# Kernel optimization log

Hardware: AMD Instinct MI355X
Metric: run time of the kernel (lower is better)

The kernel has to match this reference:

```python
import jax, jax.numpy as jnp
import numpy as np

B, N = 8, 256
IN_F, OUT_F = 64, 64
IN_E, OUT_E = 32, 64  # out_edges must equal out_features (batched matmul constraint)


def setup_inputs() -> dict:
    key = jax.random.key(0)
    ks = jax.random.split(key, 9)
    s = 0.05
    return {
        "A": jax.random.uniform(ks[0], (B, N, N), dtype=jnp.float32),
        "emb_node": jax.random.normal(ks[1], (B, N, IN_F), dtype=jnp.float32),
        "emb_edge": jax.random.normal(ks[2], (B, N, N, IN_E), dtype=jnp.float32),
        "W_node": jax.random.normal(ks[3], (IN_F, OUT_F), dtype=jnp.float32) * s,
        "b_node": jnp.zeros((OUT_F,), dtype=jnp.float32),
        "W_nodes": jax.random.normal(ks[4], (IN_F, OUT_F), dtype=jnp.float32) * s,
        "b_nodes": jnp.zeros((OUT_F,), dtype=jnp.float32),
        "W_edge": jax.random.normal(ks[5], (IN_E, OUT_E), dtype=jnp.float32) * s,
        "b_edge": jnp.zeros((OUT_E,), dtype=jnp.float32),
    }


def reference(A, emb_node, emb_edge, W_node, b_node, W_nodes, b_nodes, W_edge, b_edge):
    # Dense projections (last-axis matmul, like keras Dense)
    node_x = emb_node @ W_node + b_node        # [B,N,F]
    node_sx = emb_node @ W_nodes + b_nodes     # [B,N,F]
    edge_x = emb_edge @ W_edge + b_edge        # [B,N,N,E] (E == F)
    # Fused edge-weighted aggregation: original materializes A[...,None]*edge_x
    # then does a per-channel batched matmul with node_x; same math as:
    #   node_out[b,n,f] = sum_m A[b,n,m] * edge_x[b,n,m,f] * node_x[b,m,f]
    agg = jnp.einsum('bnm,bnmf,bmf->bnf', A, edge_x, node_x)
    node_out = jax.nn.relu(agg) + jax.nn.relu(node_sx)
    edge_out = jax.nn.relu(edge_x)
    return node_out, edge_out
```

## Files before the change

### kernel.cpp

```cpp
#include <hip/hip_runtime.h>

#define BB    8
#define NN    256
#define OUTF  64
#define INE   32

using f4 = __attribute__((ext_vector_type(4))) float;

__device__ float g_node_x[BB * NN * OUTF];
__device__ float g_relu_sx[BB * NN * OUTF];

__global__ __launch_bounds__(256) void node_proj(
    const float* __restrict__ emb_node,
    const float* __restrict__ W1, const float* __restrict__ b1,
    const float* __restrict__ W2, const float* __restrict__ b2)
{
    __shared__ float sW1[64][64];
    __shared__ float sW2[64][64];
    __shared__ float sE[4][64];

    const int tid = threadIdx.x;

    const f4* w1v = (const f4*)W1;
    const f4* w2v = (const f4*)W2;
    f4* s1 = (f4*)&sW1[0][0];
    f4* s2 = (f4*)&sW2[0][0];
#pragma unroll
    for (int i = 0; i < 4; ++i) {
        s1[tid + i * 256] = w1v[tid + i * 256];
        s2[tid + i * 256] = w2v[tid + i * 256];
    }
    const int row0 = blockIdx.x * 4;
    if (tid < 64) ((f4*)&sE[0][0])[tid] = ((const f4*)(emb_node + row0 * 64))[tid];
    __syncthreads();

    const int s = tid >> 6;
    const int f = tid & 63;
    float a1 = b1[f];
    float a2 = b2[f];
#pragma unroll
    for (int k = 0; k < 64; ++k) {
        const float e = sE[s][k];
        a1 = fmaf(e, sW1[k][f], a1);
        a2 = fmaf(e, sW2[k][f], a2);
    }
    const int row = row0 + s;
    g_node_x[row * 64 + f]  = a1;
    g_relu_sx[row * 64 + f] = fmaxf(a2, 0.f);
}

__global__ __launch_bounds__(512, 6) void edge_agg(
    const float* __restrict__ A,
    const float* __restrict__ emb_edge,
    const float* __restrict__ W_edge,
    const float* __restrict__ b_edge,
    float* __restrict__ node_out,
    float* __restrict__ edge_out)
{
    __shared__ __align__(16) unsigned char smem[36864 + 8192 + 1024];
    float* sE = (float*)smem;
    float* sW = (float*)(smem + 36864);
    float (*sRed)[64] = (float (*)[64])(smem + 36864);
    float* sA = (float*)(smem + 36864 + 8192);

    const int tid = threadIdx.x;
    const int bn  = blockIdx.x;
    const int b   = bn >> 8;

    const float* embBase = emb_edge + (size_t)bn * (NN * INE);
#pragma unroll
    for (int it = 0; it < 4; ++it) {
        const int i  = tid + it * 512;
        const f4   v = __builtin_nontemporal_load(((const f4*)embBase) + i);
        const int m  = i >> 3;
        const int k4 = i & 7;
        *(f4*)&sE[m * 36 + k4 * 4] = v;
    }
    ((f4*)sW)[tid] = ((const f4*)W_edge)[tid];
    if (tid < 64) ((f4*)sA)[tid] = ((const f4*)(A + bn * NN))[tid];
    __syncthreads();

    const int fg = tid & 15;
    const int mg = tid >> 4;
    const int f0 = fg * 4;

    const f4 bias = *(const f4*)(b_edge + f0);
    float acc[8][4];
#pragma unroll
    for (int i = 0; i < 8; ++i) {
        acc[i][0] = bias.x; acc[i][1] = bias.y; acc[i][2] = bias.z; acc[i][3] = bias.w;
    }

#pragma unroll
    for (int k4 = 0; k4 < 8; ++k4) {
        f4 w[4];
#pragma unroll
        for (int kk = 0; kk < 4; ++kk)
            w[kk] = *(const f4*)&sW[(k4 * 4 + kk) * 64 + f0];
#pragma unroll
        for (int i = 0; i < 8; ++i) {
            const f4 e = *(const f4*)&sE[(mg + i * 32) * 36 + k4 * 4];
#pragma unroll
            for (int kk = 0; kk < 4; ++kk) {
                const float ev = (kk == 0) ? e.x
                               : (kk == 1) ? e.y
                               : (kk == 2) ? e.z
                                           : e.w;
                acc[i][0] = fmaf(ev, w[kk].x, acc[i][0]);
                acc[i][1] = fmaf(ev, w[kk].y, acc[i][1]);
                acc[i][2] = fmaf(ev, w[kk].z, acc[i][2]);
                acc[i][3] = fmaf(ev, w[kk].w, acc[i][3]);
            }
        }
    }

    const float* nx = g_node_x + b * (NN * OUTF);
    const size_t outBase = (size_t)bn * (NN * OUTF);
    float agg0 = 0.f, agg1 = 0.f, agg2 = 0.f, agg3 = 0.f;
#pragma unroll
    for (int i = 0; i < 8; ++i) {
        const int m = mg + i * 32;
        const float a = sA[m];
        const f4 nxv = *(const f4*)&nx[m * 64 + f0];
        f4 st;
        st.x = fmaxf(acc[i][0], 0.f);
        st.y = fmaxf(acc[i][1], 0.f);
        st.z = fmaxf(acc[i][2], 0.f);
        st.w = fmaxf(acc[i][3], 0.f);
        __builtin_nontemporal_store(st, (f4*)&edge_out[outBase + (size_t)m * 64 + f0]);
        agg0 = fmaf(a * acc[i][0], nxv.x, agg0);
        agg1 = fmaf(a * acc[i][1], nxv.y, agg1);
        agg2 = fmaf(a * acc[i][2], nxv.z, agg2);
        agg3 = fmaf(a * acc[i][3], nxv.w, agg3);
    }

    __syncthreads();
    f4 aggv; aggv.x = agg0; aggv.y = agg1; aggv.z = agg2; aggv.w = agg3;
    *(f4*)&sRed[mg][f0] = aggv;
    __syncthreads();

    if (tid < 64) {
        float s = 0.f;
#pragma unroll
        for (int g = 0; g < 32; ++g) s += sRed[g][tid];
        node_out[bn * 64 + tid] = fmaxf(s, 0.f) + g_relu_sx[bn * 64 + tid];
    }
}

extern "C" void kernel_launch(void* const* d_in, const int* in_sizes, int n_in,
                              void* d_out, int out_size, void* d_ws, size_t ws_size,
                              hipStream_t stream) {
    const float* A        = (const float*)d_in[0];
    const float* emb_node = (const float*)d_in[1];
    const float* emb_edge = (const float*)d_in[2];
    const float* W_node   = (const float*)d_in[3];
    const float* b_node   = (const float*)d_in[4];
    const float* W_nodes  = (const float*)d_in[5];
    const float* b_nodes  = (const float*)d_in[6];
    const float* W_edge   = (const float*)d_in[7];
    const float* b_edge   = (const float*)d_in[8];

    float* node_out = (float*)d_out;
    float* edge_out = node_out + BB * NN * OUTF;

    node_proj<<<(BB * NN) / 4, 256, 0, stream>>>(emb_node, W_node, b_node, W_nodes, b_nodes);
    edge_agg<<<BB * NN, 512, 0, stream>>>(A, emb_edge, W_edge, b_edge, node_out, edge_out);
}
```

Measured before the change: 52.81 us.

## Software-pipeline edge tile loads across two rows per block; batch node_proj rows

The edge kernel now processes two (b,n) rows per 256-thread block in four half-row tiles. It register-prefetches the next tile of emb_edge and A while computing the current one, so global loads overlap with the FMA work. The cross-group reduction uses wavefront shuffles plus a small shared buffer. node_proj computes 16 rows per block to reuse weight loads. The trade-offs are fewer blocks and extra barriers, plus more register pressure from the prefetch registers.

Result: slower. 96.52 us (+82.8%).

```diff
diff --git a/kernel.cpp b/kernel.cpp
--- a/kernel.cpp
+++ b/kernel.cpp
@@ -9,6 +9,13 @@
 
 __device__ float g_node_x[BB * NN * OUTF];
 __device__ float g_relu_sx[BB * NN * OUTF];
+
+static __device__ __forceinline__ f4 relu4(f4 v) {
+    f4 r;
+    r.x = fmaxf(v.x, 0.f); r.y = fmaxf(v.y, 0.f);
+    r.z = fmaxf(v.z, 0.f); r.w = fmaxf(v.w, 0.f);
+    return r;
+}
 
 __global__ __launch_bounds__(256) void node_proj(
     const float* __restrict__ emb_node,
@@ -17,7 +24,7 @@
 {
     __shared__ float sW1[64][64];
     __shared__ float sW2[64][64];
-    __shared__ float sE[4][64];
+    __shared__ float sE[16][64];
 
     const int tid = threadIdx.x;
 
@@ -30,26 +37,36 @@
         s1[tid + i * 256] = w1v[tid + i * 256];
         s2[tid + i * 256] = w2v[tid + i * 256];
     }
-    const int row0 = blockIdx.x * 4;
-    if (tid < 64) ((f4*)&sE[0][0])[tid] = ((const f4*)(emb_node + row0 * 64))[tid];
+    const int row0 = blockIdx.x * 16;
+    ((f4*)&sE[0][0])[tid] = ((const f4*)(emb_node + row0 * 64))[tid];
     __syncthreads();
 
     const int s = tid >> 6;
     const int f = tid & 63;
-    float a1 = b1[f];
-    float a2 = b2[f];
+    float a1[4], a2[4];
+    const float bb1 = b1[f], bb2 = b2[f];
+#pragma unroll
+    for (int j = 0; j < 4; ++j) { a1[j] = bb1; a2[j] = bb2; }
 #pragma unroll
     for (int k = 0; k < 64; ++k) {
-        const float e = sE[s][k];
-        a1 = fmaf(e, sW1[k][f], a1);
-        a2 = fmaf(e, sW2[k][f], a2);
-    }
-    const int row = row0 + s;
-    g_node_x[row * 64 + f]  = a1;
-    g_relu_sx[row * 64 + f] = fmaxf(a2, 0.f);
-}
-
-__global__ __launch_bounds__(512, 6) void edge_agg(
+        const float w1 = sW1[k][f];
+        const float w2 = sW2[k][f];
+#pragma unroll
+        for (int j = 0; j < 4; ++j) {
+            const float e = sE[s + 4 * j][k];
+            a1[j] = fmaf(e, w1, a1[j]);
+            a2[j] = fmaf(e, w2, a2[j]);
+        }
+    }
+#pragma unroll
+    for (int j = 0; j < 4; ++j) {
+        const int row = row0 + s + 4 * j;
+        g_node_x[row * 64 + f]  = a1[j];
+        g_relu_sx[row * 64 + f] = fmaxf(a2[j], 0.f);
+    }
+}
+
+__global__ __launch_bounds__(256, 5) void edge_agg(
     const float* __restrict__ A,
     const float* __restrict__ emb_edge,
     const float* __restrict__ W_edge,
@@ -57,93 +74,131 @@
     float* __restrict__ node_out,
     float* __restrict__ edge_out)
 {
-    __shared__ __align__(16) unsigned char smem[36864 + 8192 + 1024];
-    float* sE = (float*)smem;
-    float* sW = (float*)(smem + 36864);
-    float (*sRed)[64] = (float (*)[64])(smem + 36864);
-    float* sA = (float*)(smem + 36864 + 8192);
-
-    const int tid = threadIdx.x;
-    const int bn  = blockIdx.x;
-    const int b   = bn >> 8;
-
-    const float* embBase = emb_edge + (size_t)bn * (NN * INE);
-#pragma unroll
-    for (int it = 0; it < 4; ++it) {
-        const int i  = tid + it * 512;
-        const f4   v = __builtin_nontemporal_load(((const f4*)embBase) + i);
-        const int m  = i >> 3;
-        const int k4 = i & 7;
-        *(f4*)&sE[m * 36 + k4 * 4] = v;
-    }
-    ((f4*)sW)[tid] = ((const f4*)W_edge)[tid];
-    if (tid < 64) ((f4*)sA)[tid] = ((const f4*)(A + bn * NN))[tid];
+    __shared__ __align__(16) float sE[128 * 36];
+    __shared__ __align__(16) float sW[32 * 64];
+    __shared__ float sA[256];
+    __shared__ float sRed[4][64];
+
+    const int tid  = threadIdx.x;
+    const int bn0  = blockIdx.x * 2;
+    const int b    = bn0 >> 8;
+    const int lane = tid & 63;
+    const int wv   = tid >> 6;
+    const int fg   = tid & 15;
+    const int mg   = tid >> 4;
+    const int f0   = fg * 4;
+
+    ((f4*)sW)[tid]       = ((const f4*)W_edge)[tid];
+    ((f4*)sW)[tid + 256] = ((const f4*)W_edge)[tid + 256];
+    const f4 bias = *(const f4*)(b_edge + f0);
+
+    {
+        const f4* src = (const f4*)(emb_edge + (size_t)bn0 * (NN * INE));
+        f4 p0 = __builtin_nontemporal_load(src + tid);
+        f4 p1 = __builtin_nontemporal_load(src + tid + 256);
+        f4 p2 = __builtin_nontemporal_load(src + tid + 512);
+        f4 p3 = __builtin_nontemporal_load(src + tid + 768);
+        f4 pa;
+        if (tid < 64) pa = ((const f4*)(A + (size_t)bn0 * NN))[tid];
+#pragma unroll
+        for (int j = 0; j < 4; ++j) {
+            const int i = tid + j * 256;
+            const f4 v = (j == 0) ? p0 : (j == 1) ? p1 : (j == 2) ? p2 : p3;
+            *(f4*)&sE[(i >> 3) * 36 + (i & 7) * 4] = v;
+        }
+        if (tid < 64) ((f4*)sA)[tid] = pa;
+    }
     __syncthreads();
 
-    const int fg = tid & 15;
-    const int mg = tid >> 4;
-    const int f0 = fg * 4;
-
-    const f4 bias = *(const f4*)(b_edge + f0);
-    float acc[8][4];
-#pragma unroll
-    for (int i = 0; i < 8; ++i) {
-        acc[i][0] = bias.x; acc[i][1] = bias.y; acc[i][2] = bias.z; acc[i][3] = bias.w;
-    }
-
-#pragma unroll
-    for (int k4 = 0; k4 < 8; ++k4) {
-        f4 w[4];
-#pragma unroll
-        for (int kk = 0; kk < 4; ++kk)
-            w[kk] = *(const f4*)&sW[(k4 * 4 + kk) * 64 + f0];
+    const float* nx = g_node_x + b * (NN * OUTF);
+    f4 agg; agg.x = 0.f; agg.y = 0.f; agg.z = 0.f; agg.w = 0.f;
+
+#pragma unroll
+    for (int t = 0; t < 4; ++t) {
+        const int h  = t & 1;
+        const int bn = bn0 + (t >> 1);
+
+        f4 q0, q1, q2, q3, qa;
+        if (t < 3) {
+            const int nbn = bn0 + ((t + 1) >> 1);
+            const int nh  = (t + 1) & 1;
+            const f4* nsrc = (const f4*)(emb_edge
+                             + ((size_t)nbn * NN + (size_t)nh * 128) * INE);
+            q0 = __builtin_nontemporal_load(nsrc + tid);
+            q1 = __builtin_nontemporal_load(nsrc + tid + 256);
+            q2 = __builtin_nontemporal_load(nsrc + tid + 512);
+            q3 = __builtin_nontemporal_load(nsrc + tid + 768);
+            if (t == 1 && tid < 64)
+                qa = ((const f4*)(A + (size_t)(bn0 + 1) * NN))[tid];
+        }
+
+        f4 acc[8];
+#pragma unroll
+        for (int i = 0; i < 8; ++i) acc[i] = bias;
+#pragma unroll
+        for (int k4 = 0; k4 < 8; ++k4) {
+            f4 w[4];
+#pragma unroll
+            for (int kk = 0; kk < 4; ++kk)
+                w[kk] = *(const f4*)&sW[(k4 * 4 + kk) * 64 + f0];
+#pragma unroll
+            for (int i = 0; i < 8; ++i) {
+                const f4 e = *(const f4*)&sE[(mg + i * 16) * 36 + k4 * 4];
+                acc[i] += e.x * w[0];
+                acc[i] += e.y * w[1];
+                acc[i] += e.z * w[2];
+                acc[i] += e.w * w[3];
+            }
+        }
+
+        float* eo = edge_out + (size_t)bn * (NN * OUTF);
 #pragma unroll
         for (int i = 0; i < 8; ++i) {
-            const f4 e = *(const f4*)&sE[(mg + i * 32) * 36 + k4 * 4];
-#pragma unroll
-            for (int kk = 0; kk < 4; ++kk) {
-                const float ev = (kk == 0) ? e.x
-                               : (kk == 1) ? e.y
-                               : (kk == 2) ? e.z
-                                           : e.w;
-                acc[i][0] = fmaf(ev, w[kk].x, acc[i][0]);
-                acc[i][1] = fmaf(ev, w[kk].y, acc[i][1]);
-                acc[i][2] = fmaf(ev, w[kk].z, acc[i][2]);
-                acc[i][3] = fmaf(ev, w[kk].w, acc[i][3]);
-            }
-        }
-    }
-
-    const float* nx = g_node_x + b * (NN * OUTF);
-    const size_t outBase = (size_t)bn * (NN * OUTF);
-    float agg0 = 0.f, agg1 = 0.f, agg2 = 0.f, agg3 = 0.f;
-#pragma unroll
-    for (int i = 0; i < 8; ++i) {
-        const int m = mg + i * 32;
-        const float a = sA[m];
-        const f4 nxv = *(const f4*)&nx[m * 64 + f0];
-        f4 st;
-        st.x = fmaxf(acc[i][0], 0.f);
-        st.y = fmaxf(acc[i][1], 0.f);
-        st.z = fmaxf(acc[i][2], 0.f);
-        st.w = fmaxf(acc[i][3], 0.f);
-        __builtin_nontemporal_store(st, (f4*)&edge_out[outBase + (size_t)m * 64 + f0]);
-        agg0 = fmaf(a * acc[i][0], nxv.x, agg0);
-        agg1 = fmaf(a * acc[i][1], nxv.y, agg1);
-        agg2 = fmaf(a * acc[i][2], nxv.z, agg2);
-        agg3 = fmaf(a * acc[i][3], nxv.w, agg3);
-    }
-
-    __syncthreads();
-    f4 aggv; aggv.x = agg0; aggv.y = agg1; aggv.z = agg2; aggv.w = agg3;
-    *(f4*)&sRed[mg][f0] = aggv;
-    __syncthreads();
-
-    if (tid < 64) {
-        float s = 0.f;
-#pragma unroll
-        for (int g = 0; g < 32; ++g) s += sRed[g][tid];
-        node_out[bn * 64 + tid] = fmaxf(s, 0.f) + g_relu_sx[bn * 64 + tid];
+            const int lm = mg + i * 16;
+            const int m  = h * 128 + lm;
+            const float a = sA[m];
+            const f4 nxv = *(const f4*)&nx[m * OUTF + f0];
+            const f4 v   = acc[i];
+            __builtin_nontemporal_store(relu4(v), (f4*)&eo[(size_t)m * OUTF + f0]);
+            agg.x = fmaf(a * v.x, nxv.x, agg.x);
+            agg.y = fmaf(a * v.y, nxv.y, agg.y);
+            agg.z = fmaf(a * v.z, nxv.z, agg.z);
+            agg.w = fmaf(a * v.w, nxv.w, agg.w);
+        }
+
+        if (h == 1) {
+            f4 r = agg;
+#pragma unroll
+            for (int s = 16; s < 64; s <<= 1) {
+                r.x += __shfl_xor(r.x, s);
+                r.y += __shfl_xor(r.y, s);
+                r.z += __shfl_xor(r.z, s);
+                r.w += __shfl_xor(r.w, s);
+            }
+            if (lane < 16) *(f4*)&sRed[wv][lane * 4] = r;
+        }
+        __syncthreads();
+
+        if (t < 3) {
+#pragma unroll
+            for (int j = 0; j < 4; ++j) {
+                const int i = tid + j * 256;
+                const f4 v = (j == 0) ? q0 : (j == 1) ? q1 : (j == 2) ? q2 : q3;
+                *(f4*)&sE[(i >> 3) * 36 + (i & 7) * 4] = v;
+            }
+            if (t == 1 && tid < 64) ((f4*)sA)[tid] = qa;
+        }
+        __syncthreads();
+
+        if (h == 1) {
+            if (tid < 64) {
+                const float s = sRed[0][tid] + sRed[1][tid]
+                              + sRed[2][tid] + sRed[3][tid];
+                node_out[bn * OUTF + tid] = fmaxf(s, 0.f)
+                                          + g_relu_sx[bn * OUTF + tid];
+            }
+            agg.x = 0.f; agg.y = 0.f; agg.z = 0.f; agg.w = 0.f;
+        }
     }
 }
 
@@ -163,6 +218,8 @@
     float* node_out = (float*)d_out;
     float* edge_out = node_out + BB * NN * OUTF;
 
-    node_proj<<<(BB * NN) / 4, 256, 0, stream>>>(emb_node, W_node, b_node, W_nodes, b_nodes);
-    edge_agg<<<BB * NN, 512, 0, stream>>>(A, emb_edge, W_edge, b_edge, node_out, edge_out);
-}
+    node_proj<<<(BB * NN) / 16, 256, 0, stream>>>(emb_node, W_node, b_node,
+                                                  W_nodes, b_nodes);
+    edge_agg<<<(BB * NN) / 2, 256, 0, stream>>>(A, emb_edge, W_edge, b_edge,
+                                                node_out, edge_out);
+}
```
